# Performance work log

Hardware: AMD Instinct MI355X
Metric: run time of the kernel (lower is better)

## Reference

```python
import jax, jax.numpy as jnp
import numpy as np

HID = 2048; H = 16; QLR = 1536; KVLR = 512
DN = 128   # qk_nope_head_dim
DR = 64    # qk_rope_head_dim
DV = 128   # v_head_dim
EPS = 1e-6
B, S = 2, 2048


def rmsnorm(x):
    return x * jax.lax.rsqrt(jnp.mean(x * x, axis=-1, keepdims=True) + EPS)


def rope_tables(seq_len):
    inv_freq = 1.0 / (10000.0 ** (jnp.arange(0, DR, 2, dtype=jnp.float32) / DR))  # [DR/2]
    ang = jnp.arange(seq_len, dtype=jnp.float32)[:, None] * inv_freq[None, :]     # [S, DR/2]
    cos = jnp.concatenate([jnp.cos(ang), jnp.cos(ang)], axis=-1)                  # [S, DR]
    sin = jnp.concatenate([jnp.sin(ang), jnp.sin(ang)], axis=-1)
    return cos, sin


def apply_rope(x, cos, sin):
    # x: [B, h, S, DR]; half-split rotation
    half = DR // 2
    rh = jnp.concatenate([-x[..., half:], x[..., :half]], axis=-1)
    return x * cos + rh * sin


def setup_inputs() -> dict:
    key = jax.random.key(0)
    ks = jax.random.split(key, 7)
    w = 0.02
    inp = {
        "X": jax.random.normal(ks[0], (B, S, HID), dtype=jnp.float32),
        "attention_mask": jnp.tril(jnp.ones((S, S), dtype=jnp.int32)),
        "Wq_down": jax.random.normal(ks[1], (HID, QLR), dtype=jnp.float32) * w,
        "bq_down": jnp.zeros((QLR,), dtype=jnp.float32),
        "Wq_up": jax.random.normal(ks[2], (QLR, H * (DN + DR)), dtype=jnp.float32) * w,
        "bq_up": jnp.zeros((H * (DN + DR),), dtype=jnp.float32),
        "Wkv_down": jax.random.normal(ks[3], (HID, DR + KVLR), dtype=jnp.float32) * w,
        "bkv_down": jnp.zeros((DR + KVLR,), dtype=jnp.float32),
        "Wkv_up": jax.random.normal(ks[4], (KVLR, H * (DN + DV)), dtype=jnp.float32) * w,
        "bkv_up": jnp.zeros((H * (DN + DV),), dtype=jnp.float32),
        "Wo": jax.random.normal(ks[5], (H * DV, HID), dtype=jnp.float32) * w,
        "bo": jnp.zeros((HID,), dtype=jnp.float32),
    }
    return inp


def reference(X, attention_mask, Wq_down, bq_down, Wq_up, bq_up,
              Wkv_down, bkv_down, Wkv_up, bkv_up, Wo, bo):
    b, s, _ = X.shape
    # query path: low-rank down -> RMSNorm -> up
    q = rmsnorm(X @ Wq_down + bq_down) @ Wq_up + bq_up            # [B,S,H*(DN+DR)]
    q = q.reshape(b, s, H, DN + DR).transpose(0, 2, 1, 3)          # [B,H,S,DN+DR]
    q_nope, q_rope = q[..., :DN], q[..., DN:]
    # kv path: shared rope key + compressed latent
    ckv = X @ Wkv_down + bkv_down                                  # [B,S,DR+KVLR]
    k_rope = ckv[..., :DR].reshape(b, s, 1, DR).transpose(0, 2, 1, 3)  # [B,1,S,DR]
    kv = rmsnorm(ckv[..., DR:]) @ Wkv_up + bkv_up                  # [B,S,H*(DN+DV)]
    kv = kv.reshape(b, s, H, DN + DV).transpose(0, 2, 1, 3)        # [B,H,S,DN+DV]
    k_nope, value = kv[..., :DN], kv[..., DN:]
    # decoupled RoPE
    cos, sin = rope_tables(s)
    q_rope = apply_rope(q_rope, cos, sin)
    k_rope = apply_rope(k_rope, cos, sin)
    query = jnp.concatenate([q_nope, q_rope], axis=-1)             # [B,H,S,DN+DR]
    key = jnp.concatenate([k_nope, jnp.broadcast_to(k_rope, (b, H, s, DR))], axis=-1)
    # attention (manual matmul -> mask -> softmax -> matmul; dropout p=0)
    scale = 1.0 / np.sqrt(DN + DR)
    scores = jnp.einsum('bhqd,bhkd->bhqk', query, key) * scale     # [B,H,S,S]
    scores = jnp.where(attention_mask[None, None, :, :] == 0, -jnp.inf, scores)
    probs = jax.nn.softmax(scores, axis=-1)
    attn = jnp.einsum('bhqk,bhkd->bhqd', probs, value)             # [B,H,S,DV]
    attn = attn.transpose(0, 2, 1, 3).reshape(b, s, H * DV)
    return attn @ Wo + bo
```

## Files before the change

### kernel.cpp

```cpp
#include <hip/hip_runtime.h>

#define HID 2048
#define NH 16
#define QLR 1536
#define KVLR 512
#define DN 128
#define DR 64
#define DV 128
#define BB 2
#define SS 2048
#define NTOK (BB*SS)
#define QD 3072
#define KVD 4096
#define CKVD 576
#define NQT (SS/64)

typedef __bf16 bf16x8 __attribute__((ext_vector_type(8)));
typedef float f32x4 __attribute__((ext_vector_type(4)));
typedef unsigned short us4v __attribute__((ext_vector_type(4)));

__device__ __forceinline__ unsigned short f2bf(float f){
  unsigned u = __builtin_bit_cast(unsigned, f);
  return (unsigned short)((u + 0x7fffu + ((u>>16)&1u)) >> 16);
}
__device__ __forceinline__ float bf2f(unsigned short h){
  unsigned u = ((unsigned)h)<<16; return __builtin_bit_cast(float, u);
}
__device__ __forceinline__ unsigned cvt_pk_bf16(float a, float b){
  unsigned r;
  asm("v_cvt_pk_bf16_f32 %0, %1, %2" : "=v"(r) : "v"(a), "v"(b));
  return r;
}

#define GLOAD16(g, l) __builtin_amdgcn_global_load_lds( \
    (const __attribute__((address_space(1))) void*)(const void*)(g), \
    (__attribute__((address_space(3))) void*)(void*)(l), 16, 0, 0)

__global__ void cvt_f32_bf16(const float* __restrict__ in, unsigned short* __restrict__ out, int n4){
  int i = blockIdx.x*256 + threadIdx.x;
  if (i < n4){
    float4 v = ((const float4*)in)[i];
    us4v o = { f2bf(v.x), f2bf(v.y), f2bf(v.z), f2bf(v.w) };
    ((us4v*)out)[i] = o;
  }
}

__global__ void wtrans(const float* __restrict__ W, unsigned short* __restrict__ WT,
                       int K, int N){
  __shared__ float t[32][33];
  int n0 = blockIdx.x*32, k0 = blockIdx.y*32;
  int tx = threadIdx.x & 31, ty = threadIdx.x >> 5;
  #pragma unroll
  for (int i = ty; i < 32; i += 8){
    int k = k0 + i, n = n0 + tx;
    t[i][tx] = (n < N) ? W[(size_t)k*N + n] : 0.f;
  }
  __syncthreads();
  #pragma unroll
  for (int i = ty; i < 32; i += 8){
    int n = n0 + i, k = k0 + tx;
    WT[(size_t)n*K + k] = f2bf(t[tx][i]);
  }
}

template<bool OUTF32>
__device__ __forceinline__ void gemm_core(
  unsigned short* As, unsigned short* Bs,
  const unsigned short* __restrict__ A, int lda,
  const unsigned short* __restrict__ BT,
  const float* __restrict__ bias,
  void* __restrict__ Cv, int ldc,
  int N, int K, int bx, int by)
{
  const int tid = threadIdx.x;
  const int wave = tid>>6, lane = tid&63, lq = lane&15, lg = lane>>4;
  const int tm = by*128, tn = bx*128;
  const int wm = (wave>>1)*64, wn = (wave&1)*64;
  f32x4 acc[4][4] = {};
  char* AsB = (char*)As; char* BsB = (char*)Bs;
  const int r8 = tid>>3;
  const int sc = ((tid&7) ^ (r8&7))*8;
  for (int kt = 0; kt < K; kt += 64){
    __syncthreads();
    #pragma unroll
    for (int rd=0; rd<4; rd++){
      GLOAD16(A  + (size_t)(tm + rd*32 + r8)*lda + kt + sc, AsB + rd*4096 + wave*1024);
      GLOAD16(BT + (size_t)(tn + rd*32 + r8)*K   + kt + sc, BsB + rd*4096 + wave*1024);
    }
    asm volatile("s_waitcnt vmcnt(0)" ::: "memory");
    __syncthreads();
    #pragma unroll
    for (int h=0; h<2; h++){
      bf16x8 af[4], bfr[4];
      #pragma unroll
      for (int i=0;i<4;i++) af[i]  = *(const bf16x8*)(AsB + (wm+16*i+lq)*128 + ((((h*4+lg)^(lq&7)))<<4));
      #pragma unroll
      for (int j=0;j<4;j++) bfr[j] = *(const bf16x8*)(BsB + (wn+16*j+lq)*128 + ((((h*4+lg)^(lq&7)))<<4));
      #pragma unroll
      for (int i=0;i<4;i++)
        #pragma unroll
        for (int j=0;j<4;j++)
          acc[i][j] = __builtin_amdgcn_mfma_f32_16x16x32_bf16(af[i], bfr[j], acc[i][j], 0,0,0);
    }
  }
  #pragma unroll
  for (int i=0;i<4;i++){
    #pragma unroll
    for (int j=0;j<4;j++){
      int col = tn + wn + 16*j + lq;
      if (col < N){
        float bv = bias ? bias[col] : 0.f;
        #pragma unroll
        for (int r=0;r<4;r++){
          int row = tm + wm + 16*i + lg*4 + r;
          float v = acc[i][j][r] + bv;
          if (OUTF32) ((float*)Cv)[(size_t)row*ldc + col] = v;
          else ((unsigned short*)Cv)[(size_t)row*ldc + col] = f2bf(v);
        }
      }
    }
  }
}

__device__ __forceinline__ void xcd_remap(int& bx, int& by){
  int nwg = gridDim.x*gridDim.y;
  int lin = blockIdx.y*gridDim.x + blockIdx.x;
  int wg = (lin&7)*(nwg>>3) + (lin>>3);
  bx = wg % gridDim.x; by = wg / gridDim.x;
}

template<bool OUTF32>
__global__ __launch_bounds__(256) void gemm_bt(
  const unsigned short* __restrict__ A, int lda,
  const unsigned short* __restrict__ BT,
  const float* __restrict__ bias,
  void* __restrict__ Cv, int ldc, int N, int K)
{
  __shared__ unsigned short As[128*64];
  __shared__ unsigned short Bs[128*64];
  int bx, by; xcd_remap(bx, by);
  gemm_core<OUTF32>(As, Bs, A, lda, BT, bias, Cv, ldc, N, K, bx, by);
}

__global__ __launch_bounds__(256) void gemm_bt_dual(
  const unsigned short* __restrict__ A0, int lda0, const unsigned short* __restrict__ BT0,
  const float* __restrict__ b0, void* __restrict__ C0, int ldc0, int N0, int K0,
  const unsigned short* __restrict__ A1, int lda1, const unsigned short* __restrict__ BT1,
  const float* __restrict__ b1, void* __restrict__ C1, int ldc1, int N1, int K1,
  int split)
{
  __shared__ unsigned short As[128*64];
  __shared__ unsigned short Bs[128*64];
  int bx, by; xcd_remap(bx, by);
  if (bx < split)
    gemm_core<false>(As, Bs, A0, lda0, BT0, b0, C0, ldc0, N0, K0, bx, by);
  else
    gemm_core<false>(As, Bs, A1, lda1, BT1, b1, C1, ldc1, N1, K1, bx - split, by);
}

__device__ __forceinline__ void rms_row(unsigned short* x, int D, float* red){
  int tid = threadIdx.x;
  float ss = 0.f;
  for (int i = tid; i < D; i += 256){ float v = bf2f(x[i]); ss += v*v; }
  #pragma unroll
  for (int o=32;o;o>>=1) ss += __shfl_xor(ss, o, 64);
  if ((tid&63)==0) red[tid>>6] = ss;
  __syncthreads();
  float tot = red[0]+red[1]+red[2]+red[3];
  float sc = rsqrtf(tot/(float)D + 1e-6f);
  for (int i = tid; i < D; i += 256) x[i] = f2bf(bf2f(x[i])*sc);
}

__global__ void norms_fused(unsigned short* __restrict__ cq,
                            unsigned short* __restrict__ ckv,
                            unsigned short* __restrict__ kr){
  __shared__ float red[4];
  int bid = blockIdx.x;
  if (bid < NTOK){
    rms_row(cq + (size_t)bid*QLR, QLR, red);
  } else if (bid < 2*NTOK){
    rms_row(ckv + (size_t)(bid-NTOK)*CKVD + DR, KVLR, red);
  } else {
    int idx = (bid - 2*NTOK)*256 + threadIdx.x;
    int j = idx & 31;
    int t = idx >> 5;
    int s = t & (SS-1);
    const unsigned short* src = ckv + (size_t)t*CKVD;
    float xr = bf2f(src[j]), xi = bf2f(src[j+32]);
    float freq = powf(10000.f, -(float)(2*j)/64.f);
    float ang = (float)s * freq;
    float c = cosf(ang), sn = sinf(ang);
    kr[(size_t)t*64 + j]      = f2bf(xr*c - xi*sn);
    kr[(size_t)t*64 + j + 32] = f2bf(xi*c + xr*sn);
  }
}

__global__ void ropeq_vt_fused(unsigned short* __restrict__ q,
                               const unsigned short* __restrict__ kv,
                               unsigned short* __restrict__ vT){
  int bid = blockIdx.x;
  if (bid < NTOK*NH*32/256){
    int idx = bid*256 + threadIdx.x;
    int j = idx & 31;
    int h = (idx >> 5) & 15;
    int t = idx >> 9;
    int s = t & (SS-1);
    unsigned short* base = q + (size_t)t*QD + h*(DN+DR) + DN;
    float xr = bf2f(base[j]), xi = bf2f(base[j+32]);
    float freq = powf(10000.f, -(float)(2*j)/64.f);
    float ang = (float)s * freq;
    float c = cosf(ang), sn = sinf(ang);
    base[j]    = f2bf(xr*c - xi*sn);
    base[j+32] = f2bf(xi*c + xr*sn);
  } else {
    __shared__ unsigned short t[32][33];
    int idx = bid - NTOK*NH*32/256;
    int s0 = (idx & 63)*32, d0 = ((idx>>6)&3)*32, bh = idx>>8;
    int b = bh>>4, h = bh&15;
    int tx = threadIdx.x & 31, ty = threadIdx.x >> 5;
    #pragma unroll
    for (int i = ty; i < 32; i += 8)
      t[i][tx] = kv[((size_t)(b*SS + s0+i))*KVD + h*(DN+DV) + DN + d0 + tx];
    __syncthreads();
    #pragma unroll
    for (int i = ty; i < 32; i += 8)
      vT[((size_t)(bh*DV + d0+i))*SS + s0 + tx] = t[tx][i];
  }
}

__global__ __launch_bounds__(256) void attn_kernel(
  const unsigned short* __restrict__ q,
  const unsigned short* __restrict__ kv,
  const unsigned short* __restrict__ kr,
  const unsigned short* __restrict__ vT,
  unsigned short* __restrict__ attn)
{
  __shared__ unsigned short Ksn[2][32*128];
  __shared__ unsigned short Ksr[2][32*64];
  __shared__ unsigned short Vs [2][128*32];
  __shared__ unsigned short Ps [4*512];
  const int tid = threadIdx.x, wave = tid>>6, lane = tid&63, lq = lane&15, lg = lane>>4;
  const int lin = blockIdx.x;
  const int bh = (lin&7) + 8*((lin>>3)&3);
  const int qt = NQT-1 - (lin>>5);
  const int b = bh>>4, h = bh&15;
  const float kmul = 1.44269504f * 0.07216878364f;

  const int rK = tid>>4, cK = (tid&15) ^ ((tid>>4)&7);
  const int rR = tid>>3, cR = (tid&7) ^ ((tid>>3)&7);
  const unsigned short* pKn0 = kv + (size_t)(b*SS + rK)*KVD + h*(DN+DV) + cK*8;
  const unsigned short* pKn1 = pKn0 + (size_t)16*KVD;
  const unsigned short* pKr  = kr + (size_t)(b*SS + rR)*64 + cR*8;
  const unsigned short* pV0  = vT + ((size_t)bh*DV + (tid>>2))*SS + (tid&3)*8;
  const unsigned short* pV1  = pV0 + (size_t)64*SS;

#define STAGE_ATTN(bufi) do {                                                 \
    GLOAD16(pKn0, (char*)Ksn[bufi] +        wave*1024);                       \
    GLOAD16(pKn1, (char*)Ksn[bufi] + 4096 + wave*1024);                       \
    GLOAD16(pKr,  (char*)Ksr[bufi] +        wave*1024);                       \
    GLOAD16(pV0,  (char*)Vs[bufi]  +        wave*1024);                       \
    GLOAD16(pV1,  (char*)Vs[bufi]  + 4096 + wave*1024);                       \
    pKn0 += 32*KVD; pKn1 += 32*KVD; pKr += 32*64; pV0 += 32; pV1 += 32;       \
  } while(0)

  const int qw = qt*64 + wave*16;
  const int myq = qw + lq;
  bf16x8 qf[6];
  {
    const unsigned short* qrow = q + (size_t)(b*SS + qw + lq)*QD + h*(DN+DR);
    #pragma unroll
    for (int ks=0;ks<6;ks++) qf[ks] = *(const bf16x8*)(qrow + ks*32 + lg*8);
  }
  f32x4 oacc[8] = {};
  float m = -1e30f, lsum = 0.f;
  const int nkt = 2*qt + 2;

  STAGE_ATTN(0);
  asm volatile("s_waitcnt vmcnt(0)" ::: "memory");
  __builtin_amdgcn_s_barrier();
  int cur = 0;
  for (int kt = 0; kt < nkt; kt++){
    if (kt+1 < nkt) STAGE_ATTN(cur^1);
    f32x4 sacc[2] = {};
    __builtin_amdgcn_s_setprio(1);
    #pragma unroll
    for (int jf=0;jf<2;jf++){
      const int rowb = jf*16 + lq;
      #pragma unroll
      for (int ks=0;ks<4;ks++){
        bf16x8 kf = *(const bf16x8*)((char*)Ksn[cur] + rowb*256 + ((((ks*4+lg)^(lq&7)))<<4));
        sacc[jf] = __builtin_amdgcn_mfma_f32_16x16x32_bf16(kf, qf[ks], sacc[jf], 0,0,0);
      }
      #pragma unroll
      for (int ks=0;ks<2;ks++){
        bf16x8 kf = *(const bf16x8*)((char*)Ksr[cur] + rowb*128 + ((((ks*4+lg)^(lq&7)))<<4));
        sacc[jf] = __builtin_amdgcn_mfma_f32_16x16x32_bf16(kf, qf[4+ks], sacc[jf], 0,0,0);
      }
    }
    __builtin_amdgcn_s_setprio(0);
    float sv[2][4]; float pmax = -1e30f;
    if (kt*32 + 31 <= qw){
      #pragma unroll
      for (int jf=0;jf<2;jf++)
        #pragma unroll
        for (int r=0;r<4;r++){ float s = sacc[jf][r]*kmul; sv[jf][r]=s; pmax=fmaxf(pmax,s); }
    } else {
      #pragma unroll
      for (int jf=0;jf<2;jf++)
        #pragma unroll
        for (int r=0;r<4;r++){
          int kpos = kt*32 + jf*16 + lg*4 + r;
          float s = (kpos <= myq) ? sacc[jf][r]*kmul : -1e30f;
          sv[jf][r]=s; pmax=fmaxf(pmax,s);
        }
    }
    pmax = fmaxf(pmax, __shfl_xor(pmax, 16, 64));
    pmax = fmaxf(pmax, __shfl_xor(pmax, 32, 64));
    if (!__all(pmax <= m + 8.f)){
      float mnew = fmaxf(m, pmax);
      float alpha = __builtin_amdgcn_exp2f(m - mnew);
      m = mnew;
      lsum *= alpha;
      #pragma unroll
      for (int df=0;df<8;df++)
        #pragma unroll
        for (int r=0;r<4;r++) oacc[df][r] *= alpha;
    }
    float psum = 0.f;
    #pragma unroll
    for (int jf=0;jf<2;jf++){
      float p0 = __builtin_amdgcn_exp2f(sv[jf][0] - m);
      float p1 = __builtin_amdgcn_exp2f(sv[jf][1] - m);
      float p2 = __builtin_amdgcn_exp2f(sv[jf][2] - m);
      float p3 = __builtin_amdgcn_exp2f(sv[jf][3] - m);
      psum += (p0+p1)+(p2+p3);
      uint2 pk = { cvt_pk_bf16(p0,p1), cvt_pk_bf16(p2,p3) };
      *(uint2*)((char*)Ps + wave*1024 + lq*64 + jf*32 + lg*8) = pk;
    }
    psum += __shfl_xor(psum, 16, 64);
    psum += __shfl_xor(psum, 32, 64);
    lsum += psum;
    bf16x8 pf = *(const bf16x8*)((char*)Ps + wave*1024 + lq*64 + lg*16);
    __builtin_amdgcn_s_setprio(1);
    #pragma unroll
    for (int df=0;df<8;df++){
      bf16x8 vf = *(const bf16x8*)(Vs[cur] + (df*16+lq)*32 + lg*8);
      oacc[df] = __builtin_amdgcn_mfma_f32_16x16x32_bf16(vf, pf, oacc[df], 0,0,0);
    }
    __builtin_amdgcn_s_setprio(0);
    asm volatile("s_waitcnt vmcnt(0)" ::: "memory");
    __builtin_amdgcn_s_barrier();
    cur ^= 1;
  }
  float inv = 1.f / lsum;
  #pragma unroll
  for (int df=0;df<8;df++){
    uint2 o = { cvt_pk_bf16(oacc[df][0]*inv, oacc[df][1]*inv),
                cvt_pk_bf16(oacc[df][2]*inv, oacc[df][3]*inv) };
    *(uint2*)(attn + (size_t)(b*SS + myq)*2048 + h*DV + df*16 + lg*4) = o;
  }
#undef STAGE_ATTN
}

extern "C" void kernel_launch(void* const* d_in, const int* in_sizes, int n_in,
                              void* d_out, int out_size, void* d_ws, size_t ws_size,
                              hipStream_t stream){
  const float* X    = (const float*)d_in[0];
  const float* Wqd  = (const float*)d_in[2];
  const float* bqd  = (const float*)d_in[3];
  const float* Wqu  = (const float*)d_in[4];
  const float* bqu  = (const float*)d_in[5];
  const float* Wkvd = (const float*)d_in[6];
  const float* bkvd = (const float*)d_in[7];
  const float* Wkvu = (const float*)d_in[8];
  const float* bkvu = (const float*)d_in[9];
  const float* Wo   = (const float*)d_in[10];
  const float* bo   = (const float*)d_in[11];
  float* out = (float*)d_out;

  char* ws = (char*)d_ws;
  unsigned short* Xb    = (unsigned short*)(ws + 0);
  unsigned short* attnb = (unsigned short*)(ws + 0);
  char*           arena = ws + 16777216;
  unsigned short* Wt1 = (unsigned short*)(arena);
  unsigned short* Wt3 = (unsigned short*)(arena + 6291456);
  unsigned short* Wt2 = (unsigned short*)(arena);
  unsigned short* Wt4 = (unsigned short*)(arena + 9437184);
  unsigned short* Wt5 = (unsigned short*)(arena);
  unsigned short* cq   = (unsigned short*)(ws + 31457280);
  unsigned short* qtmp = (unsigned short*)(ws + 44040192);
  unsigned short* ckv  = (unsigned short*)(ws + 69206016);
  unsigned short* kvt  = (unsigned short*)(ws + 73924608);
  unsigned short* kr   = (unsigned short*)(ws + 107479040);
  unsigned short* vT   = (unsigned short*)(ws + 108003328);

  cvt_f32_bf16<<<dim3(NTOK*HID/4/256), 256, 0, stream>>>(X, Xb, NTOK*HID/4);
  wtrans<<<dim3(QLR/32, HID/32), 256, 0, stream>>>(Wqd, Wt1, HID, QLR);
  wtrans<<<dim3(640/32, HID/32), 256, 0, stream>>>(Wkvd, Wt3, HID, CKVD);
  gemm_bt_dual<<<dim3(QLR/128 + 640/128, NTOK/128), 256, 0, stream>>>(
      Xb, HID, Wt1, bqd, cq, QLR, QLR, HID,
      Xb, HID, Wt3, bkvd, ckv, CKVD, CKVD, HID, QLR/128);
  norms_fused<<<dim3(2*NTOK + NTOK*32/256), 256, 0, stream>>>(cq, ckv, kr);
  wtrans<<<dim3(QD/32, QLR/32), 256, 0, stream>>>(Wqu, Wt2, QLR, QD);
  wtrans<<<dim3(KVD/32, KVLR/32), 256, 0, stream>>>(Wkvu, Wt4, KVLR, KVD);
  gemm_bt_dual<<<dim3(QD/128 + KVD/128, NTOK/128), 256, 0, stream>>>(
      cq, QLR, Wt2, bqu, qtmp, QD, QD, QLR,
      ckv + DR, CKVD, Wt4, bkvu, kvt, KVD, KVD, KVLR, QD/128);
  ropeq_vt_fused<<<dim3(NTOK*NH*32/256 + 8192), 256, 0, stream>>>(qtmp, kvt, vT);
  attn_kernel<<<dim3(NQT * BB*NH), 256, 0, stream>>>(qtmp, kvt, kr, vT, attnb);
  wtrans<<<dim3(HID/32, HID/32), 256, 0, stream>>>(Wo, Wt5, HID, HID);
  gemm_bt<true><<<dim3(HID/128, NTOK/128), 256, 0, stream>>>(attnb, HID, Wt5, bo, out, HID, HID, HID);
}
```

Measured before the change: 360.0 us.

## Switch attention to 32x32x16 MFMA with 128-query tiles per block

Each attention wave now handles 32 query rows with 32x32x16 bf16 MFMA instructions instead of 16 rows with 16x16x32, so a block covers 128 queries and the grid is halved. Every staged K/V tile is reused across twice as many queries, which cuts LDS and global traffic per FLOP, and a row-max shuffle is dropped. The V LDS layout gains an XOR swizzle and the P buffer is padded to cut bank conflicts. In exchange, per-thread register use rises (larger accumulators and 12 Q fragments) and there are fewer blocks, which may lower occupancy and make the causal load balance coarser.

```diff
diff --git a/kernel.cpp b/kernel.cpp
--- a/kernel.cpp
+++ b/kernel.cpp
@@ -13,11 +13,13 @@
 #define QD 3072
 #define KVD 4096
 #define CKVD 576
-#define NQT (SS/64)
+#define NQT2 (SS/128)
 
 typedef __bf16 bf16x8 __attribute__((ext_vector_type(8)));
 typedef float f32x4 __attribute__((ext_vector_type(4)));
+typedef float f32x16 __attribute__((ext_vector_type(16)));
 typedef unsigned short us4v __attribute__((ext_vector_type(4)));
+typedef unsigned int u32x4 __attribute__((ext_vector_type(4)));
 
 __device__ __forceinline__ unsigned short f2bf(float f){
   unsigned u = __builtin_bit_cast(unsigned, f);
@@ -238,20 +240,22 @@
   __shared__ unsigned short Ksn[2][32*128];
   __shared__ unsigned short Ksr[2][32*64];
   __shared__ unsigned short Vs [2][128*32];
-  __shared__ unsigned short Ps [4*512];
-  const int tid = threadIdx.x, wave = tid>>6, lane = tid&63, lq = lane&15, lg = lane>>4;
+  __shared__ unsigned short Ps [4*32*36];
+  const int tid = threadIdx.x, wave = tid>>6, lane = tid&63;
+  const int lo = lane&31, hi = lane>>5;
   const int lin = blockIdx.x;
   const int bh = (lin&7) + 8*((lin>>3)&3);
-  const int qt = NQT-1 - (lin>>5);
+  const int qt = NQT2-1 - (lin>>5);
   const int b = bh>>4, h = bh&15;
   const float kmul = 1.44269504f * 0.07216878364f;
 
-  const int rK = tid>>4, cK = (tid&15) ^ ((tid>>4)&7);
-  const int rR = tid>>3, cR = (tid&7) ^ ((tid>>3)&7);
+  const int rK = tid>>4, cK = (tid&15) ^ (rK&7);
+  const int rR = tid>>3, cR = (tid&7) ^ (rR&7);
+  const int rV = tid>>2, cV = (tid&3) ^ (rV&3);
   const unsigned short* pKn0 = kv + (size_t)(b*SS + rK)*KVD + h*(DN+DV) + cK*8;
   const unsigned short* pKn1 = pKn0 + (size_t)16*KVD;
   const unsigned short* pKr  = kr + (size_t)(b*SS + rR)*64 + cR*8;
-  const unsigned short* pV0  = vT + ((size_t)bh*DV + (tid>>2))*SS + (tid&3)*8;
+  const unsigned short* pV0  = vT + ((size_t)bh*DV + rV)*SS + cV*8;
   const unsigned short* pV1  = pV0 + (size_t)64*SS;
 
 #define STAGE_ATTN(bufi) do {                                                 \
@@ -263,17 +267,17 @@
     pKn0 += 32*KVD; pKn1 += 32*KVD; pKr += 32*64; pV0 += 32; pV1 += 32;       \
   } while(0)
 
-  const int qw = qt*64 + wave*16;
-  const int myq = qw + lq;
-  bf16x8 qf[6];
+  const int qw = qt*128 + wave*32;
+  const int myq = qw + lo;
+  bf16x8 qf[12];
   {
-    const unsigned short* qrow = q + (size_t)(b*SS + qw + lq)*QD + h*(DN+DR);
-    #pragma unroll
-    for (int ks=0;ks<6;ks++) qf[ks] = *(const bf16x8*)(qrow + ks*32 + lg*8);
-  }
-  f32x4 oacc[8] = {};
+    const unsigned short* qrow = q + (size_t)(b*SS + myq)*QD + h*(DN+DR);
+    #pragma unroll
+    for (int c=0;c<12;c++) qf[c] = *(const bf16x8*)(qrow + c*16 + hi*8);
+  }
+  f32x16 oacc[4] = {};
   float m = -1e30f, lsum = 0.f;
-  const int nkt = 2*qt + 2;
+  const int nkt = 4*qt + 4;
 
   STAGE_ATTN(0);
   asm volatile("s_waitcnt vmcnt(0)" ::: "memory");
@@ -281,71 +285,70 @@
   int cur = 0;
   for (int kt = 0; kt < nkt; kt++){
     if (kt+1 < nkt) STAGE_ATTN(cur^1);
-    f32x4 sacc[2] = {};
+    f32x16 sacc = {};
     __builtin_amdgcn_s_setprio(1);
     #pragma unroll
-    for (int jf=0;jf<2;jf++){
-      const int rowb = jf*16 + lq;
-      #pragma unroll
-      for (int ks=0;ks<4;ks++){
-        bf16x8 kf = *(const bf16x8*)((char*)Ksn[cur] + rowb*256 + ((((ks*4+lg)^(lq&7)))<<4));
-        sacc[jf] = __builtin_amdgcn_mfma_f32_16x16x32_bf16(kf, qf[ks], sacc[jf], 0,0,0);
+    for (int ck=0;ck<8;ck++){
+      bf16x8 kf = *(const bf16x8*)((char*)Ksn[cur] + lo*256 + ((((ck*2+hi)^(lo&7)))<<4));
+      sacc = __builtin_amdgcn_mfma_f32_32x32x16_bf16(kf, qf[ck], sacc, 0,0,0);
+    }
+    #pragma unroll
+    for (int ck=0;ck<4;ck++){
+      bf16x8 kf = *(const bf16x8*)((char*)Ksr[cur] + lo*128 + ((((ck*2+hi)^(lo&7)))<<4));
+      sacc = __builtin_amdgcn_mfma_f32_32x32x16_bf16(kf, qf[8+ck], sacc, 0,0,0);
+    }
+    __builtin_amdgcn_s_setprio(0);
+    float s[16]; float pmax = -1e30f;
+    if (kt*32 + 31 <= qw){
+      #pragma unroll
+      for (int r=0;r<16;r++){ float v = sacc[r]*kmul; s[r]=v; pmax=fmaxf(pmax,v); }
+    } else {
+      #pragma unroll
+      for (int r=0;r<16;r++){
+        int kpos = kt*32 + (r&3) + 8*(r>>2) + 4*hi;
+        float v = (kpos <= myq) ? sacc[r]*kmul : -1e30f;
+        s[r]=v; pmax=fmaxf(pmax,v);
       }
-      #pragma unroll
-      for (int ks=0;ks<2;ks++){
-        bf16x8 kf = *(const bf16x8*)((char*)Ksr[cur] + rowb*128 + ((((ks*4+lg)^(lq&7)))<<4));
-        sacc[jf] = __builtin_amdgcn_mfma_f32_16x16x32_bf16(kf, qf[4+ks], sacc[jf], 0,0,0);
-      }
-    }
-    __builtin_amdgcn_s_setprio(0);
-    float sv[2][4]; float pmax = -1e30f;
-    if (kt*32 + 31 <= qw){
-      #pragma unroll
-      for (int jf=0;jf<2;jf++)
-        #pragma unroll
-        for (int r=0;r<4;r++){ float s = sacc[jf][r]*kmul; sv[jf][r]=s; pmax=fmaxf(pmax,s); }
-    } else {
-      #pragma unroll
-      for (int jf=0;jf<2;jf++)
-        #pragma unroll
-        for (int r=0;r<4;r++){
-          int kpos = kt*32 + jf*16 + lg*4 + r;
-          float s = (kpos <= myq) ? sacc[jf][r]*kmul : -1e30f;
-          sv[jf][r]=s; pmax=fmaxf(pmax,s);
-        }
-    }
-    pmax = fmaxf(pmax, __shfl_xor(pmax, 16, 64));
+    }
     pmax = fmaxf(pmax, __shfl_xor(pmax, 32, 64));
     if (!__all(pmax <= m + 8.f)){
       float mnew = fmaxf(m, pmax);
       float alpha = __builtin_amdgcn_exp2f(m - mnew);
-      m = mnew;
-      lsum *= alpha;
-      #pragma unroll
-      for (int df=0;df<8;df++)
+      m = mnew; lsum *= alpha;
+      #pragma unroll
+      for (int dt=0;dt<4;dt++)
         #pragma unroll
-        for (int r=0;r<4;r++) oacc[df][r] *= alpha;
+        for (int r=0;r<16;r++) oacc[dt][r] *= alpha;
     }
     float psum = 0.f;
     #pragma unroll
-    for (int jf=0;jf<2;jf++){
-      float p0 = __builtin_amdgcn_exp2f(sv[jf][0] - m);
-      float p1 = __builtin_amdgcn_exp2f(sv[jf][1] - m);
-      float p2 = __builtin_amdgcn_exp2f(sv[jf][2] - m);
-      float p3 = __builtin_amdgcn_exp2f(sv[jf][3] - m);
-      psum += (p0+p1)+(p2+p3);
-      uint2 pk = { cvt_pk_bf16(p0,p1), cvt_pk_bf16(p2,p3) };
-      *(uint2*)((char*)Ps + wave*1024 + lq*64 + jf*32 + lg*8) = pk;
-    }
-    psum += __shfl_xor(psum, 16, 64);
+    for (int r=0;r<16;r++){ s[r] = __builtin_amdgcn_exp2f(s[r] - m); psum += s[r]; }
     psum += __shfl_xor(psum, 32, 64);
     lsum += psum;
-    bf16x8 pf = *(const bf16x8*)((char*)Ps + wave*1024 + lq*64 + lg*16);
+    unsigned short* Pw = Ps + wave*32*36;
+    #pragma unroll
+    for (int rg=0; rg<4; rg++){
+      uint2 pk = { cvt_pk_bf16(s[rg*4+0], s[rg*4+1]),
+                   cvt_pk_bf16(s[rg*4+2], s[rg*4+3]) };
+      *(uint2*)((char*)Pw + lo*72 + rg*16 + hi*8) = pk;
+    }
+    bf16x8 pf[2];
+    #pragma unroll
+    for (int j=0;j<2;j++){
+      uint2 a0 = *(const uint2*)((char*)Pw + lo*72 + (2*j+hi)*16);
+      uint2 a1 = *(const uint2*)((char*)Pw + lo*72 + (2*j+hi)*16 + 8);
+      u32x4 pk4 = { a0.x, a0.y, a1.x, a1.y };
+      pf[j] = __builtin_bit_cast(bf16x8, pk4);
+    }
     __builtin_amdgcn_s_setprio(1);
     #pragma unroll
-    for (int df=0;df<8;df++){
-      bf16x8 vf = *(const bf16x8*)(Vs[cur] + (df*16+lq)*32 + lg*8);
-      oacc[df] = __builtin_amdgcn_mfma_f32_16x16x32_bf16(vf, pf, oacc[df], 0,0,0);
+    for (int dt=0; dt<4; dt++){
+      const int row = dt*32 + lo;
+      #pragma unroll
+      for (int j=0;j<2;j++){
+        bf16x8 vf = *(const bf16x8*)((char*)Vs[cur] + row*64 + ((((j*2+hi)^(lo&3)))<<4));
+        oacc[dt] = __builtin_amdgcn_mfma_f32_32x32x16_bf16(vf, pf[j], oacc[dt], 0,0,0);
+      }
     }
     __builtin_amdgcn_s_setprio(0);
     asm volatile("s_waitcnt vmcnt(0)" ::: "memory");
@@ -353,11 +356,16 @@
     cur ^= 1;
   }
   float inv = 1.f / lsum;
+  unsigned short* orow = attn + (size_t)(b*SS + myq)*2048 + h*DV;
   #pragma unroll
-  for (int df=0;df<8;df++){
-    uint2 o = { cvt_pk_bf16(oacc[df][0]*inv, oacc[df][1]*inv),
-                cvt_pk_bf16(oacc[df][2]*inv, oacc[df][3]*inv) };
-    *(uint2*)(attn + (size_t)(b*SS + myq)*2048 + h*DV + df*16 + lg*4) = o;
+  for (int dt=0; dt<4; dt++){
+    #pragma unroll
+    for (int rq=0; rq<4; rq++){
+      int dbase = dt*32 + rq*8 + hi*4;
+      uint2 o = { cvt_pk_bf16(oacc[dt][rq*4+0]*inv, oacc[dt][rq*4+1]*inv),
+                  cvt_pk_bf16(oacc[dt][rq*4+2]*inv, oacc[dt][rq*4+3]*inv) };
+      *(uint2*)(orow + dbase) = o;
+    }
   }
 #undef STAGE_ATTN
 }
@@ -407,7 +415,7 @@
       cq, QLR, Wt2, bqu, qtmp, QD, QD, QLR,
       ckv + DR, CKVD, Wt4, bkvu, kvt, KVD, KVD, KVLR, QD/128);
   ropeq_vt_fused<<<dim3(NTOK*NH*32/256 + 8192), 256, 0, stream>>>(qtmp, kvt, vT);
-  attn_kernel<<<dim3(NQT * BB*NH), 256, 0, stream>>>(qtmp, kvt, kr, vT, attnb);
+  attn_kernel<<<dim3(NQT2 * BB*NH), 256, 0, stream>>>(qtmp, kvt, kr, vT, attnb);
   wtrans<<<dim3(HID/32, HID/32), 256, 0, stream>>>(Wo, Wt5, HID, HID);
   gemm_bt<true><<<dim3(HID/128, NTOK/128), 256, 0, stream>>>(attnb, HID, Wt5, bo, out, HID, HID, HID);
 }
```

Measured after the change: 361.1 us. Within noise of the previous version (+0.3%).
